# Optimization experiments

Measured on AMD Instinct MI355X. Metric: run time of the kernel, lower is better.

Reference implementation:

```python
import jax, jax.numpy as jnp
import numpy as np

K = 16
ITERS = 5
DIST_CHUNK = 8  # feature-chunk size to avoid materializing [B,F,S,S]


def pairwise_l1(x):
    """x: [B, F, S] -> d: [B, S, S], d[b,i,j] = ||x[b,:,i]-x[b,:,j]||_1.
    Computed in feature chunks via scan so peak intermediate is [B,CH,S,S]."""
    B, F, S = x.shape
    xc = x.reshape(B, F // DIST_CHUNK, DIST_CHUNK, S).transpose(1, 0, 2, 3)  # [F/CH,B,CH,S]

    def step(acc, blk):  # blk: [B, CH, S]
        return acc + jnp.abs(blk[:, :, :, None] - blk[:, :, None, :]).sum(axis=1), None

    d, _ = jax.lax.scan(step, jnp.zeros((B, S, S), x.dtype), xc)
    return d


def kmedoids_pool(x, w):
    B, F, S = x.shape
    wm = jnp.mean(w, axis=1)                       # [B,S] per-token attention weight
    d = pairwise_l1(x)                             # [B,S,S]
    _, ctr = jax.lax.top_k(wm, K)                  # [B,K] initial medoids
    dw = d * wm[:, None, :]                        # d[b,i,j]*w[b,j]
    for _ in range(ITERS):
        # distance from every token to each current medoid: [B,S,K]
        i2c = jnp.take_along_axis(d, jnp.broadcast_to(ctr[:, None, :], (B, S, K)), axis=2)
        assign = jnp.argmin(i2c, axis=2)           # [B,S] cluster assignment
        member = jax.nn.one_hot(assign, K, dtype=x.dtype)  # [B,S,K]
        # weighted within-cluster cost for candidate i in cluster k:
        # cost[b,i,k] = sum_j d[b,i,j]*w[b,j]*member[b,j,k]
        cost = jnp.einsum('bij,bjk->bik', dw, member)
        cost = jnp.where(member > 0, cost, jnp.inf)  # medoid must be a member
        ctr = jnp.argmin(cost, axis=1)             # [B,K] new medoids
    idx = jnp.broadcast_to(ctr[:, None, :], (B, F, K))
    return jnp.take_along_axis(x, idx, axis=2)     # [B,F,K]


def setup_inputs() -> dict:
    key = jax.random.key(0)
    kx, kw = jax.random.split(key)
    B, F, S = 8, 256, 1024
    x = jax.random.normal(kx, (B, F, S), dtype=jnp.float32)
    w = jax.random.uniform(kw, (B, S, S), dtype=jnp.float32)
    return {"x": x, "w": w}


def reference(x, w):
    return kmedoids_pool(x, w)
```

## Files before the change

### kernel.cpp

```cpp
#include <hip/hip_runtime.h>
#include <math.h>

#define BB 8
#define FF 256
#define SS 1024
#define KK 16
#define ITERS 5

typedef unsigned long long ull;


#define ICH 8
__global__ void wm_part_kernel(const float* __restrict__ w, float* __restrict__ part) {
    int j = blockIdx.x * 256 + threadIdx.x;
    int ic = blockIdx.y, b = blockIdx.z;
    const float* wp = w + (size_t)b * SS * SS + (size_t)ic * (SS / ICH) * SS + j;
    float s = 0.f;
#pragma unroll 16
    for (int i = 0; i < SS / ICH; ++i) s += wp[(size_t)i * SS];
    part[((size_t)ic * BB + b) * SS + j] = s;
}

#define FCD 8
#define TS 32
#define NT (SS / TS)
__device__ __forceinline__ void async_copy16(const float* g, const float* s) {
    __builtin_amdgcn_global_load_lds((const __attribute__((address_space(1))) void*)g,
                                     (__attribute__((address_space(3))) void*)s, 16, 0, 0);
}

__global__ __launch_bounds__(128, 4) void dist_kernel(const float* __restrict__ x,
                                                      float* __restrict__ d) {
    __shared__ float smem[4096];
    int tid = threadIdx.x;
    int wave = tid >> 6, lane = tid & 63;
    int b = blockIdx.y;
    int w = blockIdx.x * 2 + wave;
    int it = 0, rem = w;
    while (rem >= NT - it) { rem -= NT - it; ++it; }
    int jt = it + rem;
    int i0 = it * TS, j0 = jt * TS;
    const float* xb = x + (size_t)b * FF * SS;
    float* db = d + (size_t)b * SS * SS;
    float* wbase = smem + wave * 2048;
    int ly = lane >> 3, lx = lane & 7;
    int sFl = lane >> 3, sTk = (lane & 7) * 4;

    float acc[4][4] = {};

    auto stage = [&](int c) {
        float* A = wbase + (c & 3) * 512;
        const float* base = xb + ((size_t)c * FCD + sFl) * SS;
        async_copy16(base + i0 + sTk, A);
        async_copy16(base + j0 + sTk, A + 256);
    };
    auto compute = [&](int c) {
        const float* A = wbase + (c & 3) * 512;
        const float* B = A + 256;
#pragma unroll
        for (int f = 0; f < FCD; ++f) {
            float4 a = *(const float4*)(A + f * 32 + ly * 4);
            float4 bb = *(const float4*)(B + f * 32 + lx * 4);
            float av[4] = {a.x, a.y, a.z, a.w};
            float bv[4] = {bb.x, bb.y, bb.z, bb.w};
#pragma unroll
            for (int r = 0; r < 4; ++r)
#pragma unroll
                for (int cc = 0; cc < 4; ++cc)
                    acc[r][cc] += fabsf(av[r] - bv[cc]);
        }
    };

    stage(0); stage(1);
#pragma unroll 1
    for (int c = 0; c < FF / FCD - 2; ++c) {
        asm volatile("s_waitcnt lgkmcnt(0)" ::: "memory");
        stage(c + 2);
        asm volatile("s_waitcnt vmcnt(4)" ::: "memory");
        compute(c);
    }
    asm volatile("s_waitcnt vmcnt(2)" ::: "memory");
    compute(30);
    asm volatile("s_waitcnt vmcnt(0)" ::: "memory");
    compute(31);

#pragma unroll
    for (int r = 0; r < 4; ++r) {
        float4 v = make_float4(acc[r][0], acc[r][1], acc[r][2], acc[r][3]);
        *(float4*)&db[(size_t)(i0 + ly * 4 + r) * SS + j0 + lx * 4] = v;
    }
    if (it != jt) {
#pragma unroll
        for (int c = 0; c < 4; ++c) {
            float4 v = make_float4(acc[0][c], acc[1][c], acc[2][c], acc[3][c]);
            *(float4*)&db[(size_t)(j0 + lx * 4 + c) * SS + i0 + ly * 4] = v;
        }
    }
}

__global__ __launch_bounds__(1024) void topk_assign_kernel(const float* __restrict__ part,
                                                           float* __restrict__ wm,
                                                           const float* __restrict__ d,
                                                           int* __restrict__ assign) {
    int b = blockIdx.x;
    int tid = threadIdx.x;
    int lane = tid & 63, wv = tid >> 6;
    __shared__ ull red[16];
    __shared__ int ctr_s[KK];
    float v = 0.f;
#pragma unroll
    for (int ic = 0; ic < ICH; ++ic) v += part[((size_t)ic * BB + b) * SS + tid];
    v *= (1.0f / SS);
    wm[b * SS + tid] = v;
    ull key = (((ull)__float_as_uint(v)) << 32) | (ull)(0xFFFFFFFFu - (unsigned)tid);
    for (int k = 0; k < KK; ++k) {
        ull kk = key;
#pragma unroll
        for (int off = 32; off; off >>= 1) {
            ull o = __shfl_down(kk, off, 64);
            if (o > kk) kk = o;
        }
        if (lane == 0) red[wv] = kk;
        __syncthreads();
        if (wv == 0) {
            ull k2 = (lane < 16) ? red[lane] : 0ull;
#pragma unroll
            for (int off = 8; off; off >>= 1) {
                ull o = __shfl_down(k2, off, 64);
                if (o > k2) k2 = o;
            }
            if (lane == 0) red[0] = k2;
        }
        __syncthreads();
        ull W = red[0];
        int widx = (int)(0xFFFFFFFFu - (unsigned)(W & 0xFFFFFFFFu));
        if (tid == widx) key = 0;
        if (tid == 0) ctr_s[k] = widx;
        __syncthreads();
    }
    const float* db = d + (size_t)b * SS * SS;
    float bv = INFINITY;
    int bk = 0;
#pragma unroll
    for (int k = 0; k < KK; ++k) {
        float vv = db[(size_t)ctr_s[k] * SS + tid];
        if (vv < bv) { bv = vv; bk = k; }
    }
    assign[b * SS + tid] = bk;
}

#define RPB 8
__global__ __launch_bounds__(256) void cost_kernel(const float* __restrict__ d,
                                                   const float* __restrict__ wm,
                                                   const int* __restrict__ assign,
                                                   float* __restrict__ cost) {
    int b = blockIdx.y;
    int tid = threadIdx.x;
    int lane = tid & 63, wv = tid >> 6;
    __shared__ float wmv[SS];
    __shared__ int asg[SS];
    *(float4*)&wmv[tid * 4] = *(const float4*)&wm[b * SS + tid * 4];
    *(int4*)&asg[tid * 4] = *(const int4*)&assign[b * SS + tid * 4];
    __syncthreads();
    const float* db = d + (size_t)b * SS * SS;
#pragma unroll
    for (int r = 0; r < RPB / 4; ++r) {
        int i = blockIdx.x * RPB + wv * (RPB / 4) + r;
        int my = asg[i];
        const float* drow = db + (size_t)i * SS;
        float s = 0.f;
#pragma unroll
        for (int c = 0; c < SS / 256; ++c) {
            int j = c * 256 + lane * 4;
            float4 dv = *(const float4*)&drow[j];
            float4 wv4 = *(const float4*)&wmv[j];
            int4 a4 = *(const int4*)&asg[j];
            s += (a4.x == my) ? dv.x * wv4.x : 0.f;
            s += (a4.y == my) ? dv.y * wv4.y : 0.f;
            s += (a4.z == my) ? dv.z * wv4.z : 0.f;
            s += (a4.w == my) ? dv.w * wv4.w : 0.f;
        }
#pragma unroll
        for (int off = 32; off; off >>= 1) s += __shfl_down(s, off, 64);
        if (lane == 0) cost[b * SS + i] = s;
    }
}

__global__ __launch_bounds__(1024) void update_assign_kernel(
        const float* __restrict__ d, const float* __restrict__ cost,
        int* __restrict__ assign, const float* __restrict__ x,
        float* __restrict__ out, int last) {
    int b = blockIdx.y;
    int q = blockIdx.x;
    int tid = threadIdx.x;
    int lane = tid & 63, wv = tid >> 6;
    __shared__ float cost_s[SS];
    __shared__ int assign_s[SS];
    __shared__ int ctr_s[KK];
    __shared__ ull pk[4][256];
    cost_s[tid] = cost[b * SS + tid];
    assign_s[tid] = assign[b * SS + tid];
    __syncthreads();
    ull best = ~0ull;
    int k = wv;
    for (int c = 0; c < SS / 64; ++c) {
        int i = c * 64 + lane;
        if (assign_s[i] == k) {
            ull key = (((ull)__float_as_uint(cost_s[i])) << 32) | (unsigned)i;
            if (key < best) best = key;
        }
    }
#pragma unroll
    for (int off = 32; off; off >>= 1) {
        ull o = __shfl_down(best, off, 64);
        if (o < best) best = o;
    }
    if (lane == 0) ctr_s[k] = (best == ~0ull) ? 0 : (int)(best & 0xFFFFFFFFu);
    __syncthreads();
    const float* db = d + (size_t)b * SS * SS;
    if (!last) {
        int tok = q * 256 + (tid & 255);
        int g = tid >> 8;
        ull bk = ~0ull;
#pragma unroll
        for (int kk = 0; kk < 4; ++kk) {
            int k2 = g * 4 + kk;
            float vv = db[(size_t)ctr_s[k2] * SS + tok];
            ull key = (((ull)__float_as_uint(vv)) << 32) | (unsigned)k2;
            if (key < bk) bk = key;
        }
        pk[g][tid & 255] = bk;
        __syncthreads();
        if (tid < 256) {
            ull m = pk[0][tid];
            if (pk[1][tid] < m) m = pk[1][tid];
            if (pk[2][tid] < m) m = pk[2][tid];
            if (pk[3][tid] < m) m = pk[3][tid];
            assign[b * SS + q * 256 + tid] = (int)(m & 0xFFFFFFFFu);
        }
    } else {
        int e = q * 1024 + tid;
        int f = e / KK, k2 = e % KK;
        out[((size_t)b * FF + f) * KK + k2] = x[((size_t)b * FF + f) * SS + ctr_s[k2]];
    }
}

extern "C" void kernel_launch(void* const* d_in, const int* in_sizes, int n_in,
                              void* d_out, int out_size, void* d_ws, size_t ws_size,
                              hipStream_t stream) {
    const float* x = (const float*)d_in[0];
    const float* w = (const float*)d_in[1];
    float* out = (float*)d_out;

    char* ws = (char*)d_ws;
    float* d = (float*)ws;
    size_t off = (size_t)BB * SS * SS * sizeof(float);
    float* wm = (float*)(ws + off);   off += (size_t)BB * SS * sizeof(float);
    int* assign = (int*)(ws + off);   off += (size_t)BB * SS * sizeof(int);
    float* cost = (float*)(ws + off); off += (size_t)BB * SS * sizeof(float);
    float* part = (float*)(ws + off);

    dist_kernel<<<dim3(264, BB), 128, 0, stream>>>(x, d);
    wm_part_kernel<<<dim3(SS / 256, ICH, BB), 256, 0, stream>>>(w, part);
    topk_assign_kernel<<<BB, 1024, 0, stream>>>(part, wm, d, assign);
    for (int itr = 0; itr < ITERS; ++itr) {
        cost_kernel<<<dim3(SS / RPB, BB), 256, 0, stream>>>(d, wm, assign, cost);
        update_assign_kernel<<<dim3(4, BB), 1024, 0, stream>>>(d, cost, assign, x, out,
                                                               itr == ITERS - 1 ? 1 : 0);
    }
}
```

Baseline: 227.7 us.

## Fuse medoid update, reassignment, and cost into one per-iteration kernel

Each k-medoids iteration used to run as two kernels: a cost kernel and an update/assign kernel. These are merged into one fused kernel launched across all cost row-blocks, with assignments and costs double-buffered between ping-pong workspace arrays. Every block redundantly recomputes the medoid selection and the full reassignment, which reads the 16 medoid rows of d, so that it can continue straight into its cost rows without a grid-wide sync. This cuts launches and removes the low-parallelism update kernel from the loop, at the cost of duplicated argmin work per block. The part buffer is reused as the second ping-pong buffer.

```diff
diff --git a/kernel.cpp b/kernel.cpp
--- a/kernel.cpp
+++ b/kernel.cpp
@@ -186,6 +186,86 @@
     }
 }
 
+__global__ __launch_bounds__(256) void fused_iter_kernel(
+        const float* __restrict__ d, const float* __restrict__ wm,
+        const int* __restrict__ assign_prev, const float* __restrict__ cost_prev,
+        int* __restrict__ assign_next, float* __restrict__ cost_next) {
+    int b = blockIdx.y;
+    int ib = blockIdx.x;
+    int tid = threadIdx.x;
+    int lane = tid & 63, wv = tid >> 6;
+    __shared__ float wmv[SS];
+    __shared__ int asg[SS];
+    __shared__ float cost_s[SS];
+    __shared__ int ctr_s[KK];
+    *(float4*)&wmv[tid * 4] = *(const float4*)&wm[b * SS + tid * 4];
+    *(int4*)&asg[tid * 4] = *(const int4*)&assign_prev[b * SS + tid * 4];
+    *(float4*)&cost_s[tid * 4] = *(const float4*)&cost_prev[b * SS + tid * 4];
+    __syncthreads();
+#pragma unroll
+    for (int q = 0; q < 4; ++q) {
+        int k = wv + q * 4;
+        ull best = ~0ull;
+        for (int c = 0; c < SS / 64; ++c) {
+            int i = c * 64 + lane;
+            if (asg[i] == k) {
+                ull key = (((ull)__float_as_uint(cost_s[i])) << 32) | (unsigned)i;
+                if (key < best) best = key;
+            }
+        }
+#pragma unroll
+        for (int off = 32; off; off >>= 1) {
+            ull o = __shfl_down(best, off, 64);
+            if (o < best) best = o;
+        }
+        if (lane == 0) ctr_s[k] = (best == ~0ull) ? 0 : (int)(best & 0xFFFFFFFFu);
+    }
+    __syncthreads();
+    const float* db = d + (size_t)b * SS * SS;
+    int na[4];
+#pragma unroll
+    for (int q = 0; q < 4; ++q) {
+        int tok = q * 256 + tid;
+        ull bk = ~0ull;
+#pragma unroll
+        for (int k = 0; k < KK; ++k) {
+            float vv = db[(size_t)ctr_s[k] * SS + tok];
+            ull key = (((ull)__float_as_uint(vv)) << 32) | (unsigned)k;
+            if (key < bk) bk = key;
+        }
+        na[q] = (int)(bk & 0xFFFFFFFFu);
+    }
+    __syncthreads();
+#pragma unroll
+    for (int q = 0; q < 4; ++q) {
+        int tok = q * 256 + tid;
+        asg[tok] = na[q];
+        assign_next[b * SS + tok] = na[q];
+    }
+    __syncthreads();
+#pragma unroll
+    for (int r = 0; r < RPB / 4; ++r) {
+        int i = ib * RPB + wv * (RPB / 4) + r;
+        int my = asg[i];
+        const float* drow = db + (size_t)i * SS;
+        float s = 0.f;
+#pragma unroll
+        for (int c = 0; c < SS / 256; ++c) {
+            int j = c * 256 + lane * 4;
+            float4 dv = *(const float4*)&drow[j];
+            float4 wv4 = *(const float4*)&wmv[j];
+            int4 a4 = *(const int4*)&asg[j];
+            s += (a4.x == my) ? dv.x * wv4.x : 0.f;
+            s += (a4.y == my) ? dv.y * wv4.y : 0.f;
+            s += (a4.z == my) ? dv.z * wv4.z : 0.f;
+            s += (a4.w == my) ? dv.w * wv4.w : 0.f;
+        }
+#pragma unroll
+        for (int off = 32; off; off >>= 1) s += __shfl_down(s, off, 64);
+        if (lane == 0) cost_next[b * SS + i] = s;
+    }
+}
+
 __global__ __launch_bounds__(1024) void update_assign_kernel(
         const float* __restrict__ d, const float* __restrict__ cost,
         int* __restrict__ assign, const float* __restrict__ x,
@@ -255,17 +335,22 @@
     char* ws = (char*)d_ws;
     float* d = (float*)ws;
     size_t off = (size_t)BB * SS * SS * sizeof(float);
-    float* wm = (float*)(ws + off);   off += (size_t)BB * SS * sizeof(float);
-    int* assign = (int*)(ws + off);   off += (size_t)BB * SS * sizeof(int);
-    float* cost = (float*)(ws + off); off += (size_t)BB * SS * sizeof(float);
+    float* wm = (float*)(ws + off);    off += (size_t)BB * SS * sizeof(float);
+    int* asgA = (int*)(ws + off);      off += (size_t)BB * SS * sizeof(int);
+    float* cstA = (float*)(ws + off);  off += (size_t)BB * SS * sizeof(float);
     float* part = (float*)(ws + off);
+    int* asgB = (int*)part;
+    float* cstB = (float*)(part + (size_t)BB * SS);
 
     dist_kernel<<<dim3(264, BB), 128, 0, stream>>>(x, d);
     wm_part_kernel<<<dim3(SS / 256, ICH, BB), 256, 0, stream>>>(w, part);
-    topk_assign_kernel<<<BB, 1024, 0, stream>>>(part, wm, d, assign);
-    for (int itr = 0; itr < ITERS; ++itr) {
-        cost_kernel<<<dim3(SS / RPB, BB), 256, 0, stream>>>(d, wm, assign, cost);
-        update_assign_kernel<<<dim3(4, BB), 1024, 0, stream>>>(d, cost, assign, x, out,
-                                                               itr == ITERS - 1 ? 1 : 0);
-    }
-}
+    topk_assign_kernel<<<BB, 1024, 0, stream>>>(part, wm, d, asgA);
+    cost_kernel<<<dim3(SS / RPB, BB), 256, 0, stream>>>(d, wm, asgA, cstA);
+    for (int itr = 1; itr < ITERS; ++itr) {
+        fused_iter_kernel<<<dim3(SS / RPB, BB), 256, 0, stream>>>(d, wm, asgA, cstA,
+                                                                  asgB, cstB);
+        int* ta = asgA; asgA = asgB; asgB = ta;
+        float* tc = cstA; cstA = cstB; cstB = tc;
+    }
+    update_assign_kernel<<<dim3(4, BB), 1024, 0, stream>>>(d, cstA, asgA, x, out, 1);
+}
```

After: 247.2 us. 8.5% more time.
